# Optimization experiments

Hardware: AMD Instinct MI355X
Metric: run time of the kernel (lower is better)

The kernel has to match this reference:

```python
import jax, jax.numpy as jnp
import numpy as np

N, E = 100000, 1600000
IN, EDGE_DIM, HID, OUT, HEADS = 128, 16, 32, 32, 2


def _glorot(key, shape, scale=0.1):
    return jax.random.normal(key, shape, dtype=jnp.float32) * scale


def setup_inputs() -> dict:
    key = jax.random.key(0)
    ks = jax.random.split(key, 20)
    HC1 = HEADS * HID
    return {
        "x": jax.random.normal(ks[0], (N, IN), dtype=jnp.float32),
        "edge_index": jax.random.randint(ks[1], (2, E), 0, N, dtype=jnp.int32),
        "edge_attr": jax.random.normal(ks[2], (E, EDGE_DIM), dtype=jnp.float32),
        # layer 1 (heads=HEADS, concat=True)
        "W1l": _glorot(ks[3], (IN, HC1)), "b1l": jnp.zeros((HC1,), jnp.float32),
        "W1r": _glorot(ks[4], (IN, HC1)), "b1r": jnp.zeros((HC1,), jnp.float32),
        "W1e": _glorot(ks[5], (EDGE_DIM, HC1)),
        "att1": _glorot(ks[6], (HEADS, HID)),
        "bias1": jnp.zeros((HC1,), jnp.float32),
        # layer 2 (heads=1, concat=False)
        "W2l": _glorot(ks[7], (HC1, HID)), "b2l": jnp.zeros((HID,), jnp.float32),
        "W2r": _glorot(ks[8], (HC1, HID)), "b2r": jnp.zeros((HID,), jnp.float32),
        "W2e": _glorot(ks[9], (EDGE_DIM, HID)),
        "att2": _glorot(ks[10], (1, HID)),
        "bias2": jnp.zeros((HID,), jnp.float32),
        # final linear
        "Wlin": _glorot(ks[11], (HID, OUT)), "blin": jnp.zeros((OUT,), jnp.float32),
    }


def gatv2_layer(x, src, dst, edge_attr, Wl, bl, Wr, br, We, att, bias, H, C, concat):
    n = x.shape[0]
    xl = (x @ Wl + bl).reshape(n, H, C)   # source transform (lin_l)
    xr = (x @ Wr + br).reshape(n, H, C)   # target transform (lin_r)
    ea = (edge_attr @ We).reshape(-1, H, C)
    m = xl[src] + xr[dst] + ea                       # [E, H, C]
    e = jnp.sum(jax.nn.leaky_relu(m, 0.2) * att, axis=-1)  # [E, H]
    # segment softmax over incoming edges of each destination node
    emax = jax.ops.segment_max(e, dst, num_segments=n)
    emax = jnp.where(jnp.isfinite(emax), emax, 0.0)
    ee = jnp.exp(e - emax[dst])
    denom = jax.ops.segment_sum(ee, dst, num_segments=n)
    alpha = ee / (denom[dst] + 1e-16)                # [E, H]
    out = jax.ops.segment_sum(xl[src] * alpha[..., None], dst, num_segments=n)  # [N, H, C]
    out = out.reshape(n, H * C) if concat else out.mean(axis=1)
    return out + bias


def reference(x, edge_index, edge_attr, W1l, b1l, W1r, b1r, W1e, att1, bias1,
              W2l, b2l, W2r, b2r, W2e, att2, bias2, Wlin, blin):
    src, dst = edge_index[0], edge_index[1]
    h = jax.nn.elu(gatv2_layer(x, src, dst, edge_attr, W1l, b1l, W1r, b1r, W1e,
                               att1, bias1, HEADS, HID, True))
    h = jax.nn.elu(gatv2_layer(h, src, dst, edge_attr, W2l, b2l, W2r, b2r, W2e,
                               att2, bias2, 1, HID, False))
    return h @ Wlin + blin
```

## Files before the change

### kernel.cpp

```cpp
#include <hip/hip_runtime.h>
#include <hip/hip_fp16.h>
#include <cstdint>
#include <cstddef>


__global__ void hist_kernel(const int* __restrict__ dst, int* __restrict__ deg, int E) {
    int e = blockIdx.x * blockDim.x + threadIdx.x;
    if (e < E) atomicAdd(&deg[dst[e]], 1);
}

__global__ void scan_part(const int* __restrict__ deg, int* __restrict__ bsum, int n) {
    int tid = threadIdx.x;
    int base = blockIdx.x * 1024 + tid * 4;
    int s = 0;
#pragma unroll
    for (int j = 0; j < 4; ++j) {
        int i = base + j;
        if (i < n) s += deg[i];
    }
#pragma unroll
    for (int off = 1; off < 64; off <<= 1) s += __shfl_xor(s, off, 64);
    __shared__ int ws[4];
    if ((tid & 63) == 0) ws[tid >> 6] = s;
    __syncthreads();
    if (tid == 0) bsum[blockIdx.x] = ws[0] + ws[1] + ws[2] + ws[3];
}

__global__ void scan_mid(int* __restrict__ bsum, int* __restrict__ rowstart, int nb, int n) {
    int tid = threadIdx.x;
    int v = (tid < nb) ? bsum[tid] : 0;
    int incl = v;
#pragma unroll
    for (int off = 1; off < 64; off <<= 1) {
        int t = __shfl_up(incl, off, 64);
        if ((tid & 63) >= off) incl += t;
    }
    __shared__ int w0;
    if (tid == 63) w0 = incl;
    __syncthreads();
    if (tid >= 64) incl += w0;
    if (tid < nb) bsum[tid] = incl - v;
    if (tid == nb - 1) rowstart[n] = incl;
}

__global__ void scan_fin(const int* __restrict__ deg, const int* __restrict__ bsum,
                         int* __restrict__ rowstart, int n) {
    int tid = threadIdx.x;
    int lane = tid & 63, wid = tid >> 6;
    int base = blockIdx.x * 1024 + tid * 4;
    int v[4];
    int s = 0;
#pragma unroll
    for (int j = 0; j < 4; ++j) {
        int i = base + j;
        v[j] = (i < n) ? deg[i] : 0;
        s += v[j];
    }
    int incl = s;
#pragma unroll
    for (int off = 1; off < 64; off <<= 1) {
        int t = __shfl_up(incl, off, 64);
        if (lane >= off) incl += t;
    }
    __shared__ int ws[4];
    if (lane == 63) ws[wid] = incl;
    __syncthreads();
    int wofs = 0;
    for (int w2 = 0; w2 < wid; ++w2) wofs += ws[w2];
    int acc = bsum[blockIdx.x] + wofs + (incl - s);
#pragma unroll
    for (int j = 0; j < 4; ++j) {
        int i = base + j;
        if (i < n) rowstart[i] = acc;
        acc += v[j];
    }
}

__global__ void scatter_kernel(const int* __restrict__ src, const int* __restrict__ dst,
                               const int* __restrict__ rowstart, int* __restrict__ cursor,
                               int2* __restrict__ es, int E) {
    int e = blockIdx.x * blockDim.x + threadIdx.x;
    if (e < E) {
        int d = dst[e];
        int p = atomicAdd(&cursor[d], 1);
        es[rowstart[d] + p] = make_int2(e, src[e]);
    }
}

__global__ void f2h_kernel(const float* __restrict__ in, __half* __restrict__ out, long n8) {
    long i = (long)blockIdx.x * blockDim.x + threadIdx.x;
    if (i < n8) {
        const float4* s = (const float4*)&in[i * 8];
        float4 a = s[0], b = s[1];
        __half2* d = (__half2*)&out[i * 8];
        d[0] = __float22half2_rn(make_float2(a.x, a.y));
        d[1] = __float22half2_rn(make_float2(a.z, a.w));
        d[2] = __float22half2_rn(make_float2(b.x, b.y));
        d[3] = __float22half2_rn(make_float2(b.z, b.w));
    }
}

__device__ __forceinline__ void fma4(float4& a, float s, const float4& wv) {
    a.x = fmaf(s, wv.x, a.x);
    a.y = fmaf(s, wv.y, a.y);
    a.z = fmaf(s, wv.z, a.z);
    a.w = fmaf(s, wv.w, a.w);
}

template <int K, int Mh, int BLOCK>
__global__ __launch_bounds__(BLOCK) void gemm_dual(
    const float* __restrict__ x,
    const float* __restrict__ Wl, const float* __restrict__ bl,
    const float* __restrict__ Wr, const float* __restrict__ br,
    __half* __restrict__ yl, __half* __restrict__ yr, int n) {
    constexpr int M = 2 * Mh;
    constexpr int MI = M / 4;
    constexpr int NG = BLOCK / MI;
    constexpr int NT = NG * 8;
    __shared__ float xs[NT * K];
    int tid = threadIdx.x;
    int node0 = blockIdx.x * NT;
    for (int i = tid * 4; i < NT * K; i += BLOCK * 4) {
        int nn = i / K, k = i % K;
        float4 v = make_float4(0.f, 0.f, 0.f, 0.f);
        if (node0 + nn < n) v = *(const float4*)&x[(size_t)(node0 + nn) * K + k];
        *(float4*)&xs[nn * K + k] = v;
    }
    __syncthreads();
    int mi = tid % MI, ng = tid / MI;
    int m0 = mi * 4, nb = ng * 8;
    const float* Wsel;
    const float* bsel;
    __half* ysel;
    int ms;
    if (m0 < Mh) { Wsel = Wl; bsel = bl; ysel = yl; ms = m0; }
    else         { Wsel = Wr; bsel = br; ysel = yr; ms = m0 - Mh; }
    float4 bias = *(const float4*)&bsel[ms];
    float4 acc[8];
#pragma unroll
    for (int nn = 0; nn < 8; ++nn) acc[nn] = bias;
    for (int k0 = 0; k0 < K; k0 += 4) {
        float4 wv0 = *(const float4*)&Wsel[(size_t)(k0 + 0) * Mh + ms];
        float4 wv1 = *(const float4*)&Wsel[(size_t)(k0 + 1) * Mh + ms];
        float4 wv2 = *(const float4*)&Wsel[(size_t)(k0 + 2) * Mh + ms];
        float4 wv3 = *(const float4*)&Wsel[(size_t)(k0 + 3) * Mh + ms];
#pragma unroll
        for (int nn = 0; nn < 8; ++nn) {
            float4 xv = *(const float4*)&xs[(nb + nn) * K + k0];
            fma4(acc[nn], xv.x, wv0);
            fma4(acc[nn], xv.y, wv1);
            fma4(acc[nn], xv.z, wv2);
            fma4(acc[nn], xv.w, wv3);
        }
    }
#pragma unroll
    for (int nn = 0; nn < 8; ++nn) {
        int node = node0 + nb + nn;
        if (node < n) {
            __half2* o = (__half2*)&ysel[(size_t)node * Mh + ms];
            o[0] = __float22half2_rn(make_float2(acc[nn].x, acc[nn].y));
            o[1] = __float22half2_rn(make_float2(acc[nn].z, acc[nn].w));
        }
    }
}

template <int K, int M, int NPB>
__global__ void linear_kernel(const float* __restrict__ x, const float* __restrict__ W,
                              const float* __restrict__ b, float* __restrict__ y, int n) {
    __shared__ float sx[NPB * K];
    int tid = threadIdx.x;
    int node0 = blockIdx.x * NPB;
    for (int i = tid; i < NPB * K; i += NPB * M) {
        int nn = node0 + i / K;
        sx[i] = (nn < n) ? x[(size_t)nn * K + (i % K)] : 0.f;
    }
    __syncthreads();
    int ln = tid / M, m = tid % M;
    int node = node0 + ln;
    if (node >= n) return;
    float acc = b[m];
#pragma unroll
    for (int k = 0; k < K; ++k) acc = fmaf(sx[ln * K + k], W[k * M + m], acc);
    y[(size_t)node * M + m] = acc;
}

template <int H, int C>
__global__ __launch_bounds__(256) void fused_edge_agg(
    const int* __restrict__ rowstart, const int2* __restrict__ es,
    const __half* __restrict__ eah,
    const float* __restrict__ We,
    const float* __restrict__ att,
    const __half* __restrict__ xl, const __half* __restrict__ xr,
    const float* __restrict__ bias, float* __restrict__ out, int n) {
    constexpr int HC = H * C;
    constexpr int LPN = HC / 2;
    constexpr int NPW = 64 / LPN;
    int gt = blockIdx.x * blockDim.x + threadIdx.x;
    int wave = gt >> 6;
    int lane = threadIdx.x & 63;
    int sub = lane / LPN;
    int j = lane % LPN;
    int ch0 = 2 * j;
    int node = wave * NPW + sub;
    if (node >= n) return;
    __half2 wh[16];
#pragma unroll
    for (int k = 0; k < 16; ++k) wh[k] = __float22half2_rn(*(const float2*)&We[k * HC + ch0]);
    float2 a2 = *(const float2*)&att[ch0];
    float2 xr2 = __half22float2(*(const __half2*)&xr[(size_t)node * HC + ch0]);
    int beg = rowstart[node], end = rowstart[node + 1];
    float denom = 0.f, acc0 = 0.f, acc1 = 0.f;

    auto edge_mv = [&](int pp, float& m0, float& m1, float2& xlf) {
        int2 e2 = es[pp];
        const float4* ea4 = (const float4*)&eah[(size_t)e2.x * 16];
        float4 r0 = ea4[0], r1 = ea4[1];
        __half2 xlh = *(const __half2*)&xl[(size_t)e2.y * HC + ch0];
        const __half2* h0 = (const __half2*)&r0;
        const __half2* h1 = (const __half2*)&r1;
        __half2 p0 = __hmul2(__low2half2(h0[0]), wh[0]);
        __half2 p1 = __hmul2(__high2half2(h0[0]), wh[1]);
        p0 = __hfma2(__low2half2(h0[1]), wh[2], p0);
        p1 = __hfma2(__high2half2(h0[1]), wh[3], p1);
        p0 = __hfma2(__low2half2(h0[2]), wh[4], p0);
        p1 = __hfma2(__high2half2(h0[2]), wh[5], p1);
        p0 = __hfma2(__low2half2(h0[3]), wh[6], p0);
        p1 = __hfma2(__high2half2(h0[3]), wh[7], p1);
        p0 = __hfma2(__low2half2(h1[0]), wh[8], p0);
        p1 = __hfma2(__high2half2(h1[0]), wh[9], p1);
        p0 = __hfma2(__low2half2(h1[1]), wh[10], p0);
        p1 = __hfma2(__high2half2(h1[1]), wh[11], p1);
        p0 = __hfma2(__low2half2(h1[2]), wh[12], p0);
        p1 = __hfma2(__high2half2(h1[2]), wh[13], p1);
        p0 = __hfma2(__low2half2(h1[3]), wh[14], p0);
        p1 = __hfma2(__high2half2(h1[3]), wh[15], p1);
        float2 mf = __half22float2(__hadd2(p0, p1));
        xlf = __half22float2(xlh);
        m0 = xlf.x + xr2.x + mf.x;
        m1 = xlf.y + xr2.y + mf.y;
    };
    auto logit = [&](float m0, float m1) -> float {
        m0 = (m0 > 0.f) ? m0 : 0.2f * m0;
        m1 = (m1 > 0.f) ? m1 : 0.2f * m1;
        float v = m0 * a2.x + m1 * a2.y;
#pragma unroll
        for (int msk = 1; msk < 16; msk <<= 1) v += __shfl_xor(v, msk, 64);
        return v;
    };

    int pp = beg;
    for (; pp + 2 <= end; pp += 2) {
        float m0a, m1a, m0b, m1b;
        float2 xla, xlb;
        edge_mv(pp, m0a, m1a, xla);
        edge_mv(pp + 1, m0b, m1b, xlb);
        float wa = __expf(logit(m0a, m1a));
        float wb = __expf(logit(m0b, m1b));
        denom += wa + wb;
        acc0 = fmaf(xla.x, wa, acc0);
        acc1 = fmaf(xla.y, wa, acc1);
        acc0 = fmaf(xlb.x, wb, acc0);
        acc1 = fmaf(xlb.y, wb, acc1);
    }
    if (pp < end) {
        float m0a, m1a;
        float2 xla;
        edge_mv(pp, m0a, m1a, xla);
        float wa = __expf(logit(m0a, m1a));
        denom += wa;
        acc0 = fmaf(xla.x, wa, acc0);
        acc1 = fmaf(xla.y, wa, acc1);
    }
    float2 b2 = *(const float2*)&bias[ch0];
    float inv = 1.f / (denom + 1e-16f);
    float o0 = acc0 * inv + b2.x;
    float o1 = acc1 * inv + b2.y;
    o0 = (o0 > 0.f) ? o0 : __expf(o0) - 1.f;
    o1 = (o1 > 0.f) ? o1 : __expf(o1) - 1.f;
    *(float2*)&out[(size_t)node * HC + ch0] = make_float2(o0, o1);
}

extern "C" void kernel_launch(void* const* d_in, const int* in_sizes, int n_in,
                              void* d_out, int out_size, void* d_ws, size_t ws_size,
                              hipStream_t stream) {
    const float* x     = (const float*)d_in[0];
    const int*   eidx  = (const int*)d_in[1];
    const float* eattr = (const float*)d_in[2];
    const float* W1l   = (const float*)d_in[3];
    const float* b1l   = (const float*)d_in[4];
    const float* W1r   = (const float*)d_in[5];
    const float* b1r   = (const float*)d_in[6];
    const float* W1e   = (const float*)d_in[7];
    const float* att1  = (const float*)d_in[8];
    const float* bias1 = (const float*)d_in[9];
    const float* W2l   = (const float*)d_in[10];
    const float* b2l   = (const float*)d_in[11];
    const float* W2r   = (const float*)d_in[12];
    const float* b2r   = (const float*)d_in[13];
    const float* W2e   = (const float*)d_in[14];
    const float* att2  = (const float*)d_in[15];
    const float* bias2 = (const float*)d_in[16];
    const float* Wlin  = (const float*)d_in[17];
    const float* blin  = (const float*)d_in[18];

    const int N = in_sizes[0] / 128;
    const int E = in_sizes[1] / 2;
    const int* src = eidx;
    const int* dst = eidx + E;

    char* p = (char*)d_ws;
    auto take = [&](size_t bytes) {
        char* r = p;
        p += (bytes + 255) & ~(size_t)255;
        return r;
    };
    int*    deg      = (int*)take((size_t)N * sizeof(int));
    int*    cursor   = (int*)take((size_t)N * sizeof(int));
    int*    rowstart = (int*)take((size_t)(N + 1) * sizeof(int));
    int*    bsum     = (int*)take(256 * sizeof(int));
    int2*   es       = (int2*)take((size_t)E * sizeof(int2));
    __half* A        = (__half*)take((size_t)N * 64 * sizeof(__half));
    __half* B        = (__half*)take((size_t)N * 64 * sizeof(__half));
    float*  Cbuf     = (float*)take((size_t)N * 64 * sizeof(float));
    __half* eah      = (__half*)take((size_t)E * 16 * sizeof(__half));

    (void)hipMemsetAsync(deg, 0, (size_t)N * sizeof(int), stream);
    (void)hipMemsetAsync(cursor, 0, (size_t)N * sizeof(int), stream);
    hist_kernel<<<(E + 255) / 256, 256, 0, stream>>>(dst, deg, E);
    {
        int nb = (N + 1023) / 1024;
        scan_part<<<nb, 256, 0, stream>>>(deg, bsum, N);
        scan_mid<<<1, 128, 0, stream>>>(bsum, rowstart, nb, N);
        scan_fin<<<nb, 256, 0, stream>>>(deg, bsum, rowstart, N);
    }
    scatter_kernel<<<(E + 255) / 256, 256, 0, stream>>>(src, dst, rowstart, cursor, es, E);
    {
        long n8 = (long)E * 16 / 8;
        f2h_kernel<<<(int)((n8 + 255) / 256), 256, 0, stream>>>(eattr, eah, n8);
    }

    gemm_dual<128, 64, 256><<<(N + 63) / 64, 256, 0, stream>>>(x, W1l, b1l, W1r, b1r, A, B, N);
    fused_edge_agg<2, 32><<<(int)(((size_t)((N + 1) / 2) * 64 + 255) / 256), 256, 0, stream>>>(
        rowstart, es, eah, W1e, att1, A, B, bias1, Cbuf, N);

    gemm_dual<64, 32, 256><<<(N + 127) / 128, 256, 0, stream>>>(Cbuf, W2l, b2l, W2r, b2r, A, B, N);
    fused_edge_agg<1, 32><<<(int)(((size_t)((N + 3) / 4) * 64 + 255) / 256), 256, 0, stream>>>(
        rowstart, es, eah, W2e, att2, A, B, bias2, Cbuf, N);

    linear_kernel<32, 32, 8><<<(N + 7) / 8, 256, 0, stream>>>(Cbuf, Wlin, blin, (float*)d_out, N);
}
```

Baseline: 468.4 us.

## Use MFMA fp16 GEMM for node transforms and batch edge loads by four

Replaces the scalar FP32 dual GEMM with an MFMA 16x16x32 f16 kernel. Weights are pre-packed into lane fragment order by a small prep kernel, and the activations are staged in shared memory as half precision. Separately, the edge aggregation loop now issues the index, edge-attribute and xl gathers for four edges before computing any of them, to raise memory-level parallelism. The GEMM inputs are rounded to fp16, and the scattered per-element half stores in the epilogue may be less coalesced.

```diff
diff --git a/kernel.cpp b/kernel.cpp
--- a/kernel.cpp
+++ b/kernel.cpp
@@ -3,6 +3,9 @@
 #include <cstdint>
 #include <cstddef>
 
+
+typedef _Float16 half8 __attribute__((ext_vector_type(8)));
+typedef float f32x4 __attribute__((ext_vector_type(4)));
 
 __global__ void hist_kernel(const int* __restrict__ dst, int* __restrict__ deg, int E) {
     int e = blockIdx.x * blockDim.x + threadIdx.x;
@@ -100,66 +103,91 @@
     }
 }
 
-__device__ __forceinline__ void fma4(float4& a, float s, const float4& wv) {
-    a.x = fmaf(s, wv.x, a.x);
-    a.y = fmaf(s, wv.y, a.y);
-    a.z = fmaf(s, wv.z, a.z);
-    a.w = fmaf(s, wv.w, a.w);
-}
-
-template <int K, int Mh, int BLOCK>
-__global__ __launch_bounds__(BLOCK) void gemm_dual(
-    const float* __restrict__ x,
-    const float* __restrict__ Wl, const float* __restrict__ bl,
-    const float* __restrict__ Wr, const float* __restrict__ br,
+template <int K, int Mh>
+__global__ void wprep_kernel(const float* __restrict__ Wl, const float* __restrict__ Wr,
+                             __half* __restrict__ Wfrag) {
+    constexpr int KS = K / 32;
+    constexpr int BN = 2 * Mh;
+    int i = blockIdx.x * blockDim.x + threadIdx.x;
+    if (i >= K * BN) return;
+    int j = i & 7;
+    int lane = (i >> 3) & 63;
+    int rest = i >> 9;
+    int ks = rest % KS;
+    int nt = rest / KS;
+    int k = ks * 32 + ((lane >> 4) & 3) * 8 + j;
+    int col = nt * 16 + (lane & 15);
+    float v = (col < Mh) ? Wl[k * Mh + col] : Wr[k * Mh + (col - Mh)];
+    Wfrag[i] = __float2half(v);
+}
+
+template <int K, int Mh, int BM>
+__global__ __launch_bounds__(256) void gemm_mfma(
+    const float* __restrict__ x, const __half* __restrict__ Wfrag,
+    const float* __restrict__ bl, const float* __restrict__ br,
     __half* __restrict__ yl, __half* __restrict__ yr, int n) {
-    constexpr int M = 2 * Mh;
-    constexpr int MI = M / 4;
-    constexpr int NG = BLOCK / MI;
-    constexpr int NT = NG * 8;
-    __shared__ float xs[NT * K];
-    int tid = threadIdx.x;
-    int node0 = blockIdx.x * NT;
-    for (int i = tid * 4; i < NT * K; i += BLOCK * 4) {
-        int nn = i / K, k = i % K;
+    constexpr int BN = 2 * Mh;
+    constexpr int KS = K / 32;
+    constexpr int NT = BN / 16;
+    constexpr int RW = BM / 64;
+    constexpr int LDP = K + 8;
+    __shared__ __half xs[BM * LDP];
+    int tid = threadIdx.x;
+    int lane = tid & 63;
+    int wave = tid >> 6;
+    int node0 = blockIdx.x * BM;
+    constexpr int ITER = (BM * K) / (256 * 4);
+#pragma unroll
+    for (int it = 0; it < ITER; ++it) {
+        int base = (it * 256 + tid) * 4;
+        int row = base / K, kk = base % K;
         float4 v = make_float4(0.f, 0.f, 0.f, 0.f);
-        if (node0 + nn < n) v = *(const float4*)&x[(size_t)(node0 + nn) * K + k];
-        *(float4*)&xs[nn * K + k] = v;
-    }
-    __syncthreads();
-    int mi = tid % MI, ng = tid / MI;
-    int m0 = mi * 4, nb = ng * 8;
-    const float* Wsel;
-    const float* bsel;
-    __half* ysel;
-    int ms;
-    if (m0 < Mh) { Wsel = Wl; bsel = bl; ysel = yl; ms = m0; }
-    else         { Wsel = Wr; bsel = br; ysel = yr; ms = m0 - Mh; }
-    float4 bias = *(const float4*)&bsel[ms];
-    float4 acc[8];
-#pragma unroll
-    for (int nn = 0; nn < 8; ++nn) acc[nn] = bias;
-    for (int k0 = 0; k0 < K; k0 += 4) {
-        float4 wv0 = *(const float4*)&Wsel[(size_t)(k0 + 0) * Mh + ms];
-        float4 wv1 = *(const float4*)&Wsel[(size_t)(k0 + 1) * Mh + ms];
-        float4 wv2 = *(const float4*)&Wsel[(size_t)(k0 + 2) * Mh + ms];
-        float4 wv3 = *(const float4*)&Wsel[(size_t)(k0 + 3) * Mh + ms];
-#pragma unroll
-        for (int nn = 0; nn < 8; ++nn) {
-            float4 xv = *(const float4*)&xs[(nb + nn) * K + k0];
-            fma4(acc[nn], xv.x, wv0);
-            fma4(acc[nn], xv.y, wv1);
-            fma4(acc[nn], xv.z, wv2);
-            fma4(acc[nn], xv.w, wv3);
-        }
-    }
-#pragma unroll
-    for (int nn = 0; nn < 8; ++nn) {
-        int node = node0 + nb + nn;
-        if (node < n) {
-            __half2* o = (__half2*)&ysel[(size_t)node * Mh + ms];
-            o[0] = __float22half2_rn(make_float2(acc[nn].x, acc[nn].y));
-            o[1] = __float22half2_rn(make_float2(acc[nn].z, acc[nn].w));
+        if (node0 + row < n) v = *(const float4*)&x[(size_t)(node0 + row) * K + kk];
+        __half2* d = (__half2*)&xs[row * LDP + kk];
+        d[0] = __float22half2_rn(make_float2(v.x, v.y));
+        d[1] = __float22half2_rn(make_float2(v.z, v.w));
+    }
+    __syncthreads();
+    f32x4 acc[RW][NT];
+#pragma unroll
+    for (int r = 0; r < RW; ++r)
+#pragma unroll
+        for (int t = 0; t < NT; ++t) {
+            f32x4 z = {0.f, 0.f, 0.f, 0.f};
+            acc[r][t] = z;
+        }
+    int r0 = lane & 15, kof = (lane >> 4) * 8;
+#pragma unroll
+    for (int ks = 0; ks < KS; ++ks) {
+        half8 a[RW];
+#pragma unroll
+        for (int r = 0; r < RW; ++r) {
+            int row = (wave * RW + r) * 16 + r0;
+            a[r] = *reinterpret_cast<const half8*>(&xs[row * LDP + ks * 32 + kof]);
+        }
+#pragma unroll
+        for (int t = 0; t < NT; ++t) {
+            half8 b = *reinterpret_cast<const half8*>(&Wfrag[(((size_t)t * KS + ks) * 64 + lane) * 8]);
+#pragma unroll
+            for (int r = 0; r < RW; ++r)
+                acc[r][t] = __builtin_amdgcn_mfma_f32_16x16x32_f16(a[r], b, acc[r][t], 0, 0, 0);
+        }
+    }
+#pragma unroll
+    for (int r = 0; r < RW; ++r) {
+#pragma unroll
+        for (int t = 0; t < NT; ++t) {
+            int col = t * 16 + (lane & 15);
+            float bv = (col < Mh) ? bl[col] : br[col - Mh];
+#pragma unroll
+            for (int q = 0; q < 4; ++q) {
+                int node = node0 + (wave * RW + r) * 16 + (lane >> 4) * 4 + q;
+                if (node < n) {
+                    float v = acc[r][t][q] + bv;
+                    if (col < Mh) yl[(size_t)node * Mh + col] = __float2half(v);
+                    else          yr[(size_t)node * Mh + (col - Mh)] = __float2half(v);
+                }
+            }
         }
     }
 }
@@ -211,11 +239,8 @@
     int beg = rowstart[node], end = rowstart[node + 1];
     float denom = 0.f, acc0 = 0.f, acc1 = 0.f;
 
-    auto edge_mv = [&](int pp, float& m0, float& m1, float2& xlf) {
-        int2 e2 = es[pp];
-        const float4* ea4 = (const float4*)&eah[(size_t)e2.x * 16];
-        float4 r0 = ea4[0], r1 = ea4[1];
-        __half2 xlh = *(const __half2*)&xl[(size_t)e2.y * HC + ch0];
+    auto gemv = [&](const float4& r0, const float4& r1, const __half2& xlh,
+                    float& m0, float& m1, float2& xlf) {
         const __half2* h0 = (const __half2*)&r0;
         const __half2* h1 = (const __half2*)&r1;
         __half2 p0 = __hmul2(__low2half2(h0[0]), wh[0]);
@@ -249,27 +274,42 @@
     };
 
     int pp = beg;
-    for (; pp + 2 <= end; pp += 2) {
-        float m0a, m1a, m0b, m1b;
-        float2 xla, xlb;
-        edge_mv(pp, m0a, m1a, xla);
-        edge_mv(pp + 1, m0b, m1b, xlb);
-        float wa = __expf(logit(m0a, m1a));
-        float wb = __expf(logit(m0b, m1b));
-        denom += wa + wb;
-        acc0 = fmaf(xla.x, wa, acc0);
-        acc1 = fmaf(xla.y, wa, acc1);
-        acc0 = fmaf(xlb.x, wb, acc0);
-        acc1 = fmaf(xlb.y, wb, acc1);
-    }
-    if (pp < end) {
-        float m0a, m1a;
-        float2 xla;
-        edge_mv(pp, m0a, m1a, xla);
-        float wa = __expf(logit(m0a, m1a));
-        denom += wa;
-        acc0 = fmaf(xla.x, wa, acc0);
-        acc1 = fmaf(xla.y, wa, acc1);
+    for (; pp + 4 <= end; pp += 4) {
+        int2 er[4];
+        float4 r0[4], r1[4];
+        __half2 xh[4];
+#pragma unroll
+        for (int u = 0; u < 4; ++u) er[u] = es[pp + u];
+#pragma unroll
+        for (int u = 0; u < 4; ++u) {
+            const float4* q = (const float4*)&eah[(size_t)er[u].x * 16];
+            r0[u] = q[0];
+            r1[u] = q[1];
+            xh[u] = *(const __half2*)&xl[(size_t)er[u].y * HC + ch0];
+        }
+#pragma unroll
+        for (int u = 0; u < 4; ++u) {
+            float m0, m1;
+            float2 xlf;
+            gemv(r0[u], r1[u], xh[u], m0, m1, xlf);
+            float w = __expf(logit(m0, m1));
+            denom += w;
+            acc0 = fmaf(xlf.x, w, acc0);
+            acc1 = fmaf(xlf.y, w, acc1);
+        }
+    }
+    for (; pp < end; ++pp) {
+        int2 e2 = es[pp];
+        const float4* q = (const float4*)&eah[(size_t)e2.x * 16];
+        float4 r0 = q[0], r1 = q[1];
+        __half2 xlh = *(const __half2*)&xl[(size_t)e2.y * HC + ch0];
+        float m0, m1;
+        float2 xlf;
+        gemv(r0, r1, xlh, m0, m1, xlf);
+        float w = __expf(logit(m0, m1));
+        denom += w;
+        acc0 = fmaf(xlf.x, w, acc0);
+        acc1 = fmaf(xlf.y, w, acc1);
     }
     float2 b2 = *(const float2*)&bias[ch0];
     float inv = 1.f / (denom + 1e-16f);
@@ -323,6 +363,8 @@
     __half* B        = (__half*)take((size_t)N * 64 * sizeof(__half));
     float*  Cbuf     = (float*)take((size_t)N * 64 * sizeof(float));
     __half* eah      = (__half*)take((size_t)E * 16 * sizeof(__half));
+    __half* Wf1      = (__half*)take((size_t)128 * 128 * sizeof(__half));
+    __half* Wf2      = (__half*)take((size_t)64 * 64 * sizeof(__half));
 
     (void)hipMemsetAsync(deg, 0, (size_t)N * sizeof(int), stream);
     (void)hipMemsetAsync(cursor, 0, (size_t)N * sizeof(int), stream);
@@ -338,12 +380,14 @@
         long n8 = (long)E * 16 / 8;
         f2h_kernel<<<(int)((n8 + 255) / 256), 256, 0, stream>>>(eattr, eah, n8);
     }
-
-    gemm_dual<128, 64, 256><<<(N + 63) / 64, 256, 0, stream>>>(x, W1l, b1l, W1r, b1r, A, B, N);
+    wprep_kernel<128, 64><<<(128 * 128 + 255) / 256, 256, 0, stream>>>(W1l, W1r, Wf1);
+    wprep_kernel<64, 32><<<(64 * 64 + 255) / 256, 256, 0, stream>>>(W2l, W2r, Wf2);
+
+    gemm_mfma<128, 64, 64><<<(N + 63) / 64, 256, 0, stream>>>(x, Wf1, b1l, b1r, A, B, N);
     fused_edge_agg<2, 32><<<(int)(((size_t)((N + 1) / 2) * 64 + 255) / 256), 256, 0, stream>>>(
         rowstart, es, eah, W1e, att1, A, B, bias1, Cbuf, N);
 
-    gemm_dual<64, 32, 256><<<(N + 127) / 128, 256, 0, stream>>>(Cbuf, W2l, b2l, W2r, b2r, A, B, N);
+    gemm_mfma<64, 32, 128><<<(N + 127) / 128, 256, 0, stream>>>(Cbuf, Wf2, b2l, b2r, A, B, N);
     fused_edge_agg<1, 32><<<(int)(((size_t)((N + 3) / 4) * 64 + 255) / 256), 256, 0, stream>>>(
         rowstart, es, eah, W2e, att2, A, B, bias2, Cbuf, N);
 
```

New measurement: 444.1 us. 5.2% less time.
